# Performance work log

Measured on AMD Instinct MI355X. Metric: run time of the kernel, lower is better.

The kernel has to match this reference:

```python
import jax, jax.numpy as jnp
import numpy as np

NEG_SLOPE = 0.01  # F.leaky_relu default


def setup_inputs() -> dict:
    key = jax.random.key(0)
    k_h, k_a, k_p, k_fc, k_at = jax.random.split(key, 5)
    N, IN_DIM, OUT_DIM, D_ACT = 1024, 256, 128, 64
    return {
        "h": jax.random.normal(k_h, (N, IN_DIM), dtype=jnp.float32),
        "action": jax.random.normal(k_a, (N, N, D_ACT), dtype=jnp.float32),
        "policy": jax.random.normal(k_p, (N, N, D_ACT), dtype=jnp.float32),
        # xavier_normal-ish scale for [OUT_DIM, IN_DIM] / [1, 2*OUT_DIM]
        "W_fc": jax.random.normal(k_fc, (OUT_DIM, IN_DIM), dtype=jnp.float32) * 0.086,
        "W_attn": jax.random.normal(k_at, (1, 2 * OUT_DIM), dtype=jnp.float32) * 0.12,
    }


def reference(h, action, policy, W_fc, W_attn):
    # z = fc(h): [N, OUT]
    z = h @ W_fc.T
    out_dim = z.shape[1]
    # attn_fc(cat([z_src, z_dst])) = z_src @ w_src + z_dst @ w_dst
    w_src = W_attn[0, :out_dim]
    w_dst = W_attn[0, out_dim:]
    s_src = z @ w_src  # [N] contribution of source node
    s_dst = z @ w_dst  # [N] contribution of destination node
    # complete graph: e[dst, src] = leaky_relu(s_src[src] + s_dst[dst])
    e = jax.nn.leaky_relu(s_dst[:, None] + s_src[None, :], NEG_SLOPE)  # [N, N]
    # segment-softmax over each node's incoming-edge mailbox (axis=1)
    alpha = jax.nn.softmax(e, axis=1)[..., None]  # [N, N, 1]
    # z = alpha * action + (1 - alpha) * policy  -> [N, N, D_ACT]
    return alpha * action + (1.0 - alpha) * policy
```

## Files before the change

### kernel.cpp

```cpp
#include <hip/hip_runtime.h>
#include <math.h>

#define NROWS 1024
#define IN_DIM 256
#define OUT_DIM 128
#define D_ACT 64
#define NEG_SLOPE 0.01f

#define NBLOCKS 2048
#define NTHREADS 256
#define STRIDE (NBLOCKS * NTHREADS)
#define TOTAL4 (NROWS * NROWS * D_ACT / 4)
#define BITERS (TOTAL4 / STRIDE)

typedef float f4 __attribute__((ext_vector_type(4)));

__global__ __launch_bounds__(256) void compute_s_kernel(
    const float* __restrict__ h,
    const float* __restrict__ W_fc,
    const float* __restrict__ W_attn,
    float* __restrict__ s_src,
    float* __restrict__ s_dst) {
  const int n = blockIdx.x;
  const int m = threadIdx.x;

  float v_src = 0.f, v_dst = 0.f;
#pragma unroll 8
  for (int k = 0; k < OUT_DIM; ++k) {
    float w = W_fc[k * IN_DIM + m];
    v_src += w * W_attn[k];
    v_dst += w * W_attn[OUT_DIM + k];
  }
  const float hv = h[n * IN_DIM + m];
  float ps = hv * v_src;
  float pd = hv * v_dst;

  for (int off = 32; off > 0; off >>= 1) {
    ps += __shfl_down(ps, off, 64);
    pd += __shfl_down(pd, off, 64);
  }
  __shared__ float sm_s[4], sm_d[4];
  const int wave = m >> 6, lane = m & 63;
  if (lane == 0) { sm_s[wave] = ps; sm_d[wave] = pd; }
  __syncthreads();
  if (m == 0) {
    s_src[n] = sm_s[0] + sm_s[1] + sm_s[2] + sm_s[3];
    s_dst[n] = sm_d[0] + sm_d[1] + sm_d[2] + sm_d[3];
  }
}

__global__ __launch_bounds__(256) void row_stats_kernel(
    const float* __restrict__ s_src,
    const float* __restrict__ s_dst,
    f4* __restrict__ rowdat) {
  const int i = blockIdx.x;
  const int t = threadIdx.x;
  const float sd = s_dst[i];

  float ev[4];
  float mx = -INFINITY;
#pragma unroll
  for (int r = 0; r < 4; ++r) {
    float e = sd + s_src[t + r * 256];
    e = e > 0.f ? e : NEG_SLOPE * e;
    ev[r] = e;
    mx = fmaxf(mx, e);
  }
  for (int off = 32; off > 0; off >>= 1) mx = fmaxf(mx, __shfl_down(mx, off, 64));

  __shared__ float sm[4];
  __shared__ float s_bcast;
  const int wave = t >> 6, lane = t & 63;
  if (lane == 0) sm[wave] = mx;
  __syncthreads();
  if (t == 0) s_bcast = fmaxf(fmaxf(sm[0], sm[1]), fmaxf(sm[2], sm[3]));
  __syncthreads();
  const float M = s_bcast;

  float sum = 0.f;
#pragma unroll
  for (int r = 0; r < 4; ++r) sum += __expf(ev[r] - M);
  for (int off = 32; off > 0; off >>= 1) sum += __shfl_down(sum, off, 64);

  __shared__ float ss[4];
  if (lane == 0) ss[wave] = sum;
  __syncthreads();
  if (t == 0) {
    f4 rd;
    rd.x = sd;
    rd.y = M;
    rd.z = 1.0f / (ss[0] + ss[1] + ss[2] + ss[3]);
    rd.w = 0.f;
    rowdat[i] = rd;
  }
}

__global__ __launch_bounds__(256) void blend_kernel(
    const f4* __restrict__ action,
    const f4* __restrict__ policy,
    const f4* __restrict__ rowdat,
    const float* __restrict__ s_src,
    f4* __restrict__ out) {
  const int base = blockIdx.x * NTHREADS + threadIdx.x;
#pragma unroll 4
  for (int k = 0; k < BITERS; ++k) {
    const int t = base + k * STRIDE;
    const int p = t >> 4;
    const int i = p >> 10;
    const int j = p & 1023;
    const f4 rd = rowdat[i];
    float e = rd.x + s_src[j];
    e = e > 0.f ? e : NEG_SLOPE * e;
    const float alpha = __expf(e - rd.y) * rd.z;
    const f4 a = action[t];
    const f4 q = policy[t];
    f4 o = alpha * a + (1.f - alpha) * q;
    __builtin_nontemporal_store(o, &out[t]);
  }
}

extern "C" void kernel_launch(void* const* d_in, const int* in_sizes, int n_in,
                              void* d_out, int out_size, void* d_ws, size_t ws_size,
                              hipStream_t stream) {
  const float* h      = (const float*)d_in[0];
  const float* action = (const float*)d_in[1];
  const float* policy = (const float*)d_in[2];
  const float* W_fc   = (const float*)d_in[3];
  const float* W_attn = (const float*)d_in[4];
  float* out = (float*)d_out;

  float* s_src  = (float*)d_ws;
  float* s_dst  = s_src + NROWS;
  f4* rowdat = (f4*)(s_dst + NROWS);

  compute_s_kernel<<<NROWS, 256, 0, stream>>>(h, W_fc, W_attn, s_src, s_dst);
  row_stats_kernel<<<NROWS, 256, 0, stream>>>(s_src, s_dst, rowdat);

  blend_kernel<<<NBLOCKS, NTHREADS, 0, stream>>>(
      (const f4*)action, (const f4*)policy,
      rowdat, s_src, (f4*)out);
}
```

Before: 182.2 us.

## Tile blend kernel per row segment with alpha precomputed in shared memory

The blend kernel no longer uses a grid-stride loop. Each block now owns a contiguous segment of one output row, computes the 128 alpha values for that segment once into LDS, and streams action and policy through a software-pipelined, manually unrolled sequence of loads and stores. This removes the per-element recomputation of exp and the redundant rowdat and s_src loads, and aims to keep more loads in flight. In exchange it adds a __syncthreads and launches more blocks, and the output stores are no longer nontemporal, which may change cache behaviour.

```diff
diff --git a/kernel.cpp b/kernel.cpp
--- a/kernel.cpp
+++ b/kernel.cpp
@@ -7,11 +7,10 @@
 #define D_ACT 64
 #define NEG_SLOPE 0.01f
 
-#define NBLOCKS 2048
-#define NTHREADS 256
-#define STRIDE (NBLOCKS * NTHREADS)
-#define TOTAL4 (NROWS * NROWS * D_ACT / 4)
-#define BITERS (TOTAL4 / STRIDE)
+#define ROW_T4 (NROWS * D_ACT / 4)
+#define SEGS_PER_ROW 8
+#define SEG_T4 (ROW_T4 / SEGS_PER_ROW)
+#define SEG_PAIRS (NROWS / SEGS_PER_ROW)
 
 typedef float f4 __attribute__((ext_vector_type(4)));
 
@@ -101,22 +100,47 @@
     const f4* __restrict__ rowdat,
     const float* __restrict__ s_src,
     f4* __restrict__ out) {
-  const int base = blockIdx.x * NTHREADS + threadIdx.x;
-#pragma unroll 4
-  for (int k = 0; k < BITERS; ++k) {
-    const int t = base + k * STRIDE;
-    const int p = t >> 4;
-    const int i = p >> 10;
-    const int j = p & 1023;
-    const f4 rd = rowdat[i];
-    float e = rd.x + s_src[j];
+  const int b = blockIdx.x;
+  const int row = b >> 3;
+  const int seg = b & 7;
+  const int tid = threadIdx.x;
+
+  __shared__ float alpha_lds[SEG_PAIRS];
+  if (tid < SEG_PAIRS) {
+    const f4 rd = rowdat[row];
+    float e = rd.x + s_src[seg * SEG_PAIRS + tid];
     e = e > 0.f ? e : NEG_SLOPE * e;
-    const float alpha = __expf(e - rd.y) * rd.z;
-    const f4 a = action[t];
-    const f4 q = policy[t];
-    f4 o = alpha * a + (1.f - alpha) * q;
-    __builtin_nontemporal_store(o, &out[t]);
+    alpha_lds[tid] = __expf(e - rd.y) * rd.z;
   }
+  __syncthreads();
+
+  const long base = (long)row * ROW_T4 + (long)seg * SEG_T4 + tid;
+  const f4* __restrict__ ap = action + base;
+  const f4* __restrict__ qp = policy + base;
+  f4* __restrict__ op = out + base;
+  const int ai = tid >> 4;
+  float al;
+
+  f4 a0 = ap[0],    q0 = qp[0];
+  f4 a1 = ap[256],  q1 = qp[256];
+
+  f4 a2 = ap[512],  q2 = qp[512];
+  f4 a3 = ap[768],  q3 = qp[768];
+  al = alpha_lds[ai];       op[0]    = q0 + al * (a0 - q0);
+  al = alpha_lds[16 + ai];  op[256]  = q1 + al * (a1 - q1);
+
+  a0 = ap[1024]; q0 = qp[1024];
+  a1 = ap[1280]; q1 = qp[1280];
+  al = alpha_lds[32 + ai];  op[512]  = q2 + al * (a2 - q2);
+  al = alpha_lds[48 + ai];  op[768]  = q3 + al * (a3 - q3);
+
+  a2 = ap[1536]; q2 = qp[1536];
+  a3 = ap[1792]; q3 = qp[1792];
+  al = alpha_lds[64 + ai];  op[1024] = q0 + al * (a0 - q0);
+  al = alpha_lds[80 + ai];  op[1280] = q1 + al * (a1 - q1);
+
+  al = alpha_lds[96 + ai];  op[1536] = q2 + al * (a2 - q2);
+  al = alpha_lds[112 + ai]; op[1792] = q3 + al * (a3 - q3);
 }
 
 extern "C" void kernel_launch(void* const* d_in, const int* in_sizes, int n_in,
@@ -136,7 +160,7 @@
   compute_s_kernel<<<NROWS, 256, 0, stream>>>(h, W_fc, W_attn, s_src, s_dst);
   row_stats_kernel<<<NROWS, 256, 0, stream>>>(s_src, s_dst, rowdat);
 
-  blend_kernel<<<NBLOCKS, NTHREADS, 0, stream>>>(
+  blend_kernel<<<NROWS * SEGS_PER_ROW, 256, 0, stream>>>(
       (const f4*)action, (const f4*)policy,
       rowdat, s_src, (f4*)out);
 }
```

After: 165.4 us. -9.2%, faster.
